# Kernel tuning notes

Measured on AMD Instinct MI355X. Metric: run time of the kernel, lower is better.

The kernel has to match this reference:

```python
import jax, jax.numpy as jnp
import numpy as np

NUM_CLASSES = 5
FEATURES = 256      # self.features_num
DIRECTIONS = 10000  # self.directions_num
H = 128
W = 128
LOSS_WEIGHT = 1.0


def setup_inputs() -> dict:
    key = jax.random.key(0)
    k1, k2, k3 = jax.random.split(key, 3)
    feature = jax.random.normal(k1, (1, FEATURES, H, W), dtype=jnp.float32)
    label = jax.random.randint(k2, (1, 1, H, W), 0, NUM_CLASSES, dtype=jnp.int32)
    proj_mat = jax.random.normal(k3, (DIRECTIONS, FEATURES), dtype=jnp.float32)
    # __init__ normalizes each row to unit norm
    proj_mat = proj_mat / jnp.sqrt((proj_mat ** 2).sum(axis=1, keepdims=True))
    return {"feature": feature, "label": label, "proj_mat": proj_mat}


def _class_loss(feat2d, w, proj_mat):
    # feat2d: [F, N] features, w: [N] {0,1} mask for this class, proj_mat: [D, F]
    n = w.sum()
    n_safe = jnp.maximum(n, 1.0)
    # first/second moments over the masked pixels (detached in the original via .cpu().numpy())
    miu = (feat2d @ w) / n_safe                                  # [F]
    m2mat = ((feat2d * w[None, :]) @ feat2d.T) / n_safe          # [F, F]
    cov_eps = jnp.clip(1e-8 * 1000.0 / n_safe, 1e-8, 1e-5)
    cov = m2mat - jnp.outer(miu, miu) + cov_eps * jnp.eye(FEATURES, dtype=feat2d.dtype)
    cov = jax.lax.stop_gradient(cov)  # original computes eig on detached numpy cov
    evals, evecs = jnp.linalg.eigh(cov)  # cov symmetric -> eigh (original: np.linalg.eig + sort)
    order = jnp.argsort(evals)[::-1]
    evals = jnp.maximum(evals[order], 1e-12)
    evecs = evecs[:, order]
    # per-direction variance after projection; rows of proj_mat already unit norm
    pm = proj_mat / jnp.sqrt((proj_mat ** 2).sum(axis=1, keepdims=True))
    std = jnp.sqrt((pm ** 2) @ evals)                            # [D]
    centered = feat2d - jax.lax.stop_gradient(miu)[:, None]      # miu_curr_t is detached
    # feat_vecs = proj_mat @ (evecs.T @ centered) / std  -> [D, N], the big intermediate
    fp = ((pm @ evecs.T) @ centered) / std[:, None]
    # masked moment accumulation (only class pixels contribute)
    m2 = ((fp ** 2) @ w) / n_safe                                # [D]
    m4 = ((fp ** 4) @ w) / n_safe                                # [D]
    loss_m2 = jnp.mean((m2 - 1.0) ** 2)
    loss_kurt = jnp.mean((m4 - 3.0 * m2 ** 2) ** 2)  # Gaussian target: m4 = 3*m2^2
    active = (n > 0).astype(feat2d.dtype)
    return loss_m2, loss_kurt, active


def reference(feature, label, proj_mat):
    feat2d = feature[0].reshape(FEATURES, H * W)    # [F, N]
    lbl = label[0, 0].reshape(H * W)                # [N]
    total = jnp.zeros((), dtype=feature.dtype)
    active_num = jnp.zeros((), dtype=feature.dtype)
    for c in range(1, NUM_CLASSES):  # original skips class 0 (background)
        w = (lbl == c).astype(feature.dtype)
        lm2, lk, a = _class_loss(feat2d, w, proj_mat)
        total = total + a * (lm2 + lk)
        active_num = active_num + a
    return LOSS_WEIGHT * total / jnp.maximum(active_num, 1.0)
```

## Files before the change

kernel.cpp:

```cpp
#include <hip/hip_runtime.h>
#include <cstdint>
#include <cstddef>

#define FEAT 256
#define HWPX 16384
#define NDIR 10000
#define NCLS 4
#define BCAP 4096
#define NSWO 7
#define JTOL 4e-12f
#define NBLK_FP 157

static const size_t OFF_FEATT = 0;
static const size_t OFF_IDX   = OFF_FEATT + (size_t)HWPX*FEAT;
static const size_t OFF_CNT   = OFF_IDX + (size_t)NCLS*HWPX;
static const size_t OFF_MIU   = OFF_CNT + 64;
static const size_t OFF_MIUP  = OFF_MIU + (size_t)NCLS*FEAT;
static const size_t OFF_G     = OFF_MIUP + (size_t)32*NCLS*FEAT;
static const size_t OFF_ETS   = OFF_G + (size_t)NCLS*FEAT*FEAT;
static const size_t OFF_EVAL  = OFF_ETS + (size_t)NCLS*FEAT*FEAT;
static const size_t OFF_LPART = OFF_EVAL + (size_t)NCLS*FEAT;
static const size_t OFF_B     = OFF_LPART + (size_t)NCLS*160*2;
static const size_t OFF_XCH   = OFF_B + (size_t)NCLS*FEAT*BCAP;

#define XCH_STRIDE ((size_t)2*32*2048)
#define XCH_XQ_OFF   16384
#define XCH_CSQ_OFF  32768
#define XCH_FLG_OFF  33280

__device__ __forceinline__ float wsum64(float v){
  int x;
  x = __builtin_amdgcn_update_dpp(0, __float_as_int(v), 0x121, 0xF, 0xF, false); v += __int_as_float(x);
  x = __builtin_amdgcn_update_dpp(0, __float_as_int(v), 0x122, 0xF, 0xF, false); v += __int_as_float(x);
  x = __builtin_amdgcn_update_dpp(0, __float_as_int(v), 0x124, 0xF, 0xF, false); v += __int_as_float(x);
  x = __builtin_amdgcn_update_dpp(0, __float_as_int(v), 0x128, 0xF, 0xF, false); v += __int_as_float(x);
  float a = __int_as_float(__builtin_amdgcn_readlane(__float_as_int(v), 0));
  float b = __int_as_float(__builtin_amdgcn_readlane(__float_as_int(v), 16));
  float c = __int_as_float(__builtin_amdgcn_readlane(__float_as_int(v), 32));
  float d = __int_as_float(__builtin_amdgcn_readlane(__float_as_int(v), 48));
  return (a + b) + (c + d);
}

__device__ __forceinline__ void waitflag(int* f, int val){
  while (__hip_atomic_load(f, __ATOMIC_ACQUIRE, __HIP_MEMORY_SCOPE_AGENT) < val)
    __builtin_amdgcn_s_sleep(2);
}

__global__ __launch_bounds__(256) void k_transpose(const float* __restrict__ feat, float* __restrict__ ws){
  __shared__ float tile[32][33];
  float* featT = ws + OFF_FEATT;
  int j0 = blockIdx.x*32, f0 = blockIdx.y*32;
  int tx = threadIdx.x, ty = threadIdx.y;
  #pragma unroll
  for (int r=0;r<4;r++){
    int f = f0 + ty + r*8;
    tile[ty+r*8][tx] = feat[(size_t)f*HWPX + j0 + tx];
  }
  __syncthreads();
  #pragma unroll
  for (int r=0;r<4;r++){
    int j = j0 + ty + r*8;
    featT[(size_t)j*FEAT + f0 + tx] = tile[tx][ty+r*8];
  }
}

__global__ __launch_bounds__(256) void k_index(const int* __restrict__ lab, float* ws){
  __shared__ int sc[256];
  int* idx = (int*)(ws + OFF_IDX);
  int* cnt = (int*)(ws + OFF_CNT);
  int t = threadIdx.x;
  if (t < NCLS*16){
    int cc = t >> 4, ii = t & 15;
    ((int*)(ws + OFF_XCH + (size_t)cc*XCH_STRIDE + XCH_FLG_OFF))[ii] = 0;
  }
  int base = t*64;
  for (int c=1;c<=NCLS;c++){
    __syncthreads();
    int m = 0;
    for (int k=0;k<64;k++) m += (lab[base+k]==c) ? 1 : 0;
    sc[t] = m;
    __syncthreads();
    for (int off=1; off<256; off<<=1){
      int v = (t>=off)? sc[t-off] : 0;
      __syncthreads();
      sc[t] += v;
      __syncthreads();
    }
    int pos = sc[t] - m;
    if (t==255) cnt[c-1] = sc[255];
    int* ic = idx + (size_t)(c-1)*HWPX;
    for (int k=0;k<64;k++){
      if (lab[base+k]==c) ic[pos++] = base+k;
    }
  }
}

__global__ __launch_bounds__(256) void k_miu_part(const int* __restrict__ lab, float* ws){
  const float* featT = ws + OFF_FEATT;
  float* part = ws + OFF_MIUP;
  int f = threadIdx.x;
  int b = blockIdx.x;
  int j0 = b*512;
  float a0=0.f,a1=0.f,a2=0.f,a3=0.f;
  for (int j=j0;j<j0+512;j++){
    float v = featT[(size_t)j*FEAT + f];
    int c = lab[j];
    a0 += (c==1)? v : 0.f;
    a1 += (c==2)? v : 0.f;
    a2 += (c==3)? v : 0.f;
    a3 += (c==4)? v : 0.f;
  }
  float* pb = part + (size_t)b*NCLS*FEAT;
  pb[0*FEAT+f] = a0;
  pb[1*FEAT+f] = a1;
  pb[2*FEAT+f] = a2;
  pb[3*FEAT+f] = a3;
}

__global__ __launch_bounds__(1024) void k_miu_fin(float* ws){
  int t = threadIdx.x;
  int c = t / FEAT;
  const float* part = ws + OFF_MIUP;
  float s = 0.f;
  for (int b=0;b<32;b++) s += part[(size_t)b*NCLS*FEAT + t];
  int n = ((int*)(ws+OFF_CNT))[c];
  float nf = fmaxf((float)n, 1.f);
  ws[OFF_MIU + t] = s / nf;
}

__global__ __launch_bounds__(256) void k_cov(float* ws){
  __shared__ float Xa[32][68];
  __shared__ float Xb[32][68];
  const float* featT = ws + OFF_FEATT;
  int c = blockIdx.y;
  const int* idx = (const int*)(ws + OFF_IDX) + (size_t)c*HWPX;
  int n = ((int*)(ws+OFF_CNT))[c];
  float nf = fmaxf((float)n,1.f);
  const float* miu = ws + OFF_MIU + (size_t)c*FEAT;
  float* G = ws + OFF_G + (size_t)c*FEAT*FEAT;
  int fb = (blockIdx.x & 3)*64, gb = (blockIdx.x >> 2)*64;
  int t = threadIdx.x;
  int ti = t & 15, tj = t >> 4;
  float acc[4][4] = {};
  int jr = t >> 3;
  int s8 = (t & 7) * 8;
  int nch = (n + 31)/32;
  for (int ch=0; ch<nch; ch++){
    int jg = ch*32 + jr;
    __syncthreads();
    if (jg < n){
      int jx = idx[jg];
      const float* row = featT + (size_t)jx*FEAT;
      #pragma unroll
      for (int k=0;k<8;k++){ Xa[jr][s8+k] = row[fb+s8+k]; Xb[jr][s8+k] = row[gb+s8+k]; }
    } else {
      #pragma unroll
      for (int k=0;k<8;k++){ Xa[jr][s8+k] = 0.f; Xb[jr][s8+k] = 0.f; }
    }
    __syncthreads();
    for (int jj=0;jj<32;jj++){
      float4 av = *(const float4*)&Xa[jj][ti*4];
      float4 bv = *(const float4*)&Xb[jj][tj*4];
      float aa[4] = {av.x,av.y,av.z,av.w};
      float bb[4] = {bv.x,bv.y,bv.z,bv.w};
      #pragma unroll
      for (int ii=0; ii<4; ii++)
        #pragma unroll
        for (int j2=0; j2<4; j2++)
          acc[ii][j2] += aa[ii]*bb[j2];
    }
  }
  float eps = fminf(fmaxf(1e-5f/nf, 1e-8f), 1e-5f);
  #pragma unroll
  for (int ii=0; ii<4; ii++){
    #pragma unroll
    for (int j2=0; j2<4; j2++){
      int f = fb + ti*4 + ii, g = gb + tj*4 + j2;
      float v = acc[ii][j2]/nf - miu[f]*miu[g] + ((f==g)? eps : 0.f);
      G[(size_t)g*FEAT + f] = v;
    }
  }
}

__global__ void
__attribute__((amdgpu_flat_work_group_size(256,256), amdgpu_waves_per_eu(1)))
k_jacobi(float* ws){
  __shared__ float QS[5*2048];
  __shared__ float PX[2][3*2048];
  __shared__ float colsq[256];
  __shared__ int srt[256];
  __shared__ int inv_[256];
  int c  = blockIdx.y;
  int kg = blockIdx.x;
  float* G   = ws + OFF_G + (size_t)c*FEAT*FEAT;
  float* XCH = ws + OFF_XCH + (size_t)c*XCH_STRIDE;
  float* XP  = XCH;
  float* XQ  = XCH + XCH_XQ_OFF;
  float* csqg= XCH + XCH_CSQ_OFF;
  int*   flg = (int*)(XCH + XCH_FLG_OFF);
  int t = threadIdx.x;
  int lane = t & 63;
  int lane4 = lane*4;
  int lw = t >> 6;
  int W  = kg*4 + lw;

#define FORJ8L(M) M(0) M(1) M(2) M(3) M(4) M(5) M(6) M(7)
#define FORJ8H(M) M(8) M(9) M(10) M(11) M(12) M(13) M(14) M(15)

#define DECL(j) float C##j##x, C##j##y, C##j##z, C##j##w;
  FORJ8L(DECL)
#undef DECL
  float n0,n1,n2,n3,n4,n5,n6,n7,n8,n9,n10,n11,n12,n13,n14,n15;

  int pg = (W==0)? 31 : W;
  int qg = (W==0)? 0  : 31 - W;

  int qslot = lw;
  int freeslot = 4;
  int qbase = qslot*2048 + lane4;

#define LDP(j) { float4 v_ = *(const float4*)&G[(size_t)(pg*8+(j))*FEAT + lane4]; \
                 C##j##x=v_.x; C##j##y=v_.y; C##j##z=v_.z; C##j##w=v_.w; }
  FORJ8L(LDP)
#undef LDP
#define LDQ(j) { float4 v_ = *(const float4*)&G[(size_t)(qg*8+((j)-8))*FEAT + lane4]; \
                 *(float4*)&QS[qbase + ((j)-8)*256] = v_; }
  FORJ8H(LDQ)
#undef LDQ

#define RP(g,ax,ay,az,aw) ax=C##g##x; ay=C##g##y; az=C##g##z; aw=C##g##w;
#define WP(g,ax,ay,az,aw) C##g##x=ax; C##g##y=ay; C##g##z=az; C##g##w=aw;
#define RQ(g,ax,ay,az,aw) { const float4 q_ = *(const float4*)&QS[qbase + ((g)-8)*256]; \
                            ax=q_.x; ay=q_.y; az=q_.z; aw=q_.w; }
#define WQ(g,ax,ay,az,aw) { float4 q_; q_.x=ax; q_.y=ay; q_.z=az; q_.w=aw; \
                            *(float4*)&QS[qbase + ((g)-8)*256] = q_; }

#define NRMP(j) n##j = wsum64(C##j##x*C##j##x + C##j##y*C##j##y + C##j##z*C##j##z + C##j##w*C##j##w);
#define NRMQ(j) { float ax,ay,az,aw; RQ(j,ax,ay,az,aw) \
                  n##j = wsum64(ax*ax + ay*ay + az*az + aw*aw); }

#define ROTG(LA,SA,ga,LB,SB,gb) { \
    float ax,ay,az,aw,bx,by,bz,bw; \
    LA(ga,ax,ay,az,aw) \
    LB(gb,bx,by,bz,bw) \
    float dp = ax*bx + ay*by + az*bz + aw*bw; \
    float d = wsum64(dp); \
    float na = n##ga, nb = n##gb; \
    bool doit = (d*d > na*nb*JTOL); \
    float tau = (nb - na) * 0.5f * __builtin_amdgcn_rcpf(d); \
    float tt = copysignf(__builtin_amdgcn_rcpf(fabsf(tau) + __builtin_amdgcn_sqrtf(1.f + tau*tau)), tau); \
    float cc = __builtin_amdgcn_rsqf(1.f + tt*tt); \
    float sn = tt*cc; \
    cc = doit ? cc : 1.f; \
    sn = doit ? sn : 0.f; \
    float x_; \
    x_ = ax; ax = cc*x_ - sn*bx; bx = sn*x_ + cc*bx; \
    x_ = ay; ay = cc*x_ - sn*by; by = sn*x_ + cc*by; \
    x_ = az; az = cc*x_ - sn*bz; bz = sn*x_ + cc*bz; \
    x_ = aw; aw = cc*x_ - sn*bw; bw = sn*x_ + cc*bw; \
    float cc2 = cc*cc, sn2 = sn*sn, csd = 2.f*cc*sn*d; \
    n##ga = cc2*na - csd + sn2*nb; \
    n##gb = sn2*na + csd + cc2*nb; \
    SA(ga,ax,ay,az,aw) \
    SB(gb,bx,by,bz,bw) \
  }
#define ROT_PP(a,b) ROTG(RP,WP,a,RP,WP,b)
#define ROT_PQ(a,b) ROTG(RP,WP,a,RQ,WQ,b)
#define ROT_QQ(a,b) ROTG(RQ,WQ,a,RQ,WQ,b)

#pragma clang loop unroll(disable)
  for (int R=0; R<NSWO*31; R++){
    NRMP(0) NRMP(1) NRMP(2) NRMP(3) NRMP(4) NRMP(5) NRMP(6) NRMP(7)
    NRMQ(8) NRMQ(9) NRMQ(10) NRMQ(11) NRMQ(12) NRMQ(13) NRMQ(14) NRMQ(15)
    ROT_PQ(0,8)  ROT_PQ(1,9)  ROT_PQ(2,10) ROT_PQ(3,11) ROT_PQ(4,12) ROT_PQ(5,13) ROT_PQ(6,14) ROT_PQ(7,15)
    ROT_PQ(0,9)  ROT_PQ(1,10) ROT_PQ(2,11) ROT_PQ(3,12) ROT_PQ(4,13) ROT_PQ(5,14) ROT_PQ(6,15) ROT_PQ(7,8)
    ROT_PQ(0,10) ROT_PQ(1,11) ROT_PQ(2,12) ROT_PQ(3,13) ROT_PQ(4,14) ROT_PQ(5,15) ROT_PQ(6,8)  ROT_PQ(7,9)
    ROT_PQ(0,11) ROT_PQ(1,12) ROT_PQ(2,13) ROT_PQ(3,14) ROT_PQ(4,15) ROT_PQ(5,8)  ROT_PQ(6,9)  ROT_PQ(7,10)
    ROT_PQ(0,12) ROT_PQ(1,13) ROT_PQ(2,14) ROT_PQ(3,15) ROT_PQ(4,8)  ROT_PQ(5,9)  ROT_PQ(6,10) ROT_PQ(7,11)
    ROT_PQ(0,13) ROT_PQ(1,14) ROT_PQ(2,15) ROT_PQ(3,8)  ROT_PQ(4,9)  ROT_PQ(5,10) ROT_PQ(6,11) ROT_PQ(7,12)
    ROT_PQ(0,14) ROT_PQ(1,15) ROT_PQ(2,8)  ROT_PQ(3,9)  ROT_PQ(4,10) ROT_PQ(5,11) ROT_PQ(6,12) ROT_PQ(7,13)
    ROT_PQ(0,15) ROT_PQ(1,8)  ROT_PQ(2,9)  ROT_PQ(3,10) ROT_PQ(4,11) ROT_PQ(5,12) ROT_PQ(6,13) ROT_PQ(7,14)
    if ((R & 3) == 3){
      ROT_PP(7,0) ROT_PP(1,6) ROT_PP(2,5) ROT_PP(3,4)  ROT_QQ(15,8)  ROT_QQ(9,14)  ROT_QQ(10,13) ROT_QQ(11,12)
      ROT_PP(7,1) ROT_PP(2,0) ROT_PP(3,6) ROT_PP(4,5)  ROT_QQ(15,9)  ROT_QQ(10,8)  ROT_QQ(11,14) ROT_QQ(12,13)
      ROT_PP(7,2) ROT_PP(3,1) ROT_PP(4,0) ROT_PP(5,6)  ROT_QQ(15,10) ROT_QQ(11,9)  ROT_QQ(12,8)  ROT_QQ(13,14)
      ROT_PP(7,3) ROT_PP(4,2) ROT_PP(5,1) ROT_PP(6,0)  ROT_QQ(15,11) ROT_QQ(12,10) ROT_QQ(13,9)  ROT_QQ(14,8)
      ROT_PP(7,4) ROT_PP(5,3) ROT_PP(6,2) ROT_PP(0,1)  ROT_QQ(15,12) ROT_QQ(13,11) ROT_QQ(14,10) ROT_QQ(8,9)
      ROT_PP(7,5) ROT_PP(6,4) ROT_PP(0,3) ROT_PP(1,2)  ROT_QQ(15,13) ROT_QQ(14,12) ROT_QQ(8,11)  ROT_QQ(9,10)
      ROT_PP(7,6) ROT_PP(0,5) ROT_PP(1,4) ROT_PP(2,3)  ROT_QQ(15,14) ROT_QQ(8,13)  ROT_QQ(9,12)  ROT_QQ(10,11)
    }

    int par = R & 1;
    if (lw >= 1){
      float* px = &PX[par][(lw-1)*2048];
#define STPX(j) { float4 v_; v_.x=C##j##x; v_.y=C##j##y; v_.z=C##j##z; v_.w=C##j##w; \
                  *(float4*)&px[(j)*256 + lane4] = v_; }
      FORJ8L(STPX)
#undef STPX
    }
    if (kg == 0 && lw == 1){
      int fb_ = freeslot*2048 + lane4;
#define STF(j) { float4 v_; v_.x=C##j##x; v_.y=C##j##y; v_.z=C##j##z; v_.w=C##j##w; \
                 *(float4*)&QS[fb_ + (j)*256] = v_; }
      FORJ8L(STF)
#undef STF
    }
    if (kg >= 1 && lw == 0){
      float* xp = XP + (size_t)(kg*2+par)*2048;
#define STXP(j) { float4 v_; v_.x=C##j##x; v_.y=C##j##y; v_.z=C##j##z; v_.w=C##j##w; \
                  *(float4*)&xp[(j)*256 + lane4] = v_; }
      FORJ8L(STXP)
#undef STXP
      if (lane == 0) __hip_atomic_store(&flg[kg], R+1, __ATOMIC_RELEASE, __HIP_MEMORY_SCOPE_AGENT);
    }
    if (lw == 3){
      if (kg < 3){
        float* xq = XQ + (size_t)(kg*2+par)*2048;
#define STXQ(j) { const float4 q_ = *(const float4*)&QS[qbase + (j)*256]; \
                  *(float4*)&xq[(j)*256 + lane4] = q_; }
        FORJ8L(STXQ)
#undef STXQ
        if (lane == 0) __hip_atomic_store(&flg[4+kg], R+1, __ATOMIC_RELEASE, __HIP_MEMORY_SCOPE_AGENT);
      } else {
#define LPQ(j) { const float4 q_ = *(const float4*)&QS[qbase + (j)*256]; \
                 C##j##x=q_.x; C##j##y=q_.y; C##j##z=q_.z; C##j##w=q_.w; }
        FORJ8L(LPQ)
#undef LPQ
      }
    }
    __syncthreads();
    if (lw <= 2 && W != 0){
      const float* px = &PX[par][lw*2048];
#define LDPX(j) { float4 v_ = *(const float4*)&px[(j)*256 + lane4]; \
                  C##j##x=v_.x; C##j##y=v_.y; C##j##z=v_.z; C##j##w=v_.w; }
      FORJ8L(LDPX)
#undef LDPX
    }
    if (lw == 3 && kg < 3){
      waitflag(&flg[kg+1], R+1);
      const float* xp = XP + (size_t)((kg+1)*2+par)*2048;
#define LDXP(j) { float4 v_ = *(const float4*)&xp[(j)*256 + lane4]; \
                  C##j##x=v_.x; C##j##y=v_.y; C##j##z=v_.z; C##j##w=v_.w; }
      FORJ8L(LDXP)
#undef LDXP
    }
    if (lw == 0 && kg >= 1){
      waitflag(&flg[4+kg-1], R+1);
      const float* xq = XQ + (size_t)((kg-1)*2+par)*2048;
      int fb_ = freeslot*2048 + lane4;
#define LDXQ(j) { float4 v_ = *(const float4*)&xq[(j)*256 + lane4]; \
                  *(float4*)&QS[fb_ + (j)*256] = v_; }
      FORJ8L(LDXQ)
#undef LDXQ
    }
    qslot += 4; if (qslot >= 5) qslot -= 5;
    freeslot += 4; if (freeslot >= 5) freeslot -= 5;
    qbase = qslot*2048 + lane4;
  }

  NRMP(0) NRMP(1) NRMP(2) NRMP(3) NRMP(4) NRMP(5) NRMP(6) NRMP(7)
  NRMQ(8) NRMQ(9) NRMQ(10) NRMQ(11) NRMQ(12) NRMQ(13) NRMQ(14) NRMQ(15)
#define WCS(j) if (lane == ((j)&15)) csqg[((j)<8)? (pg*8+(j)) : (qg*8+(j)-8)] = n##j;
  FORJ8L(WCS) FORJ8H(WCS)
#undef WCS
  __syncthreads();
  if (t == 0) __hip_atomic_fetch_add(&flg[8], 1, __ATOMIC_ACQ_REL, __HIP_MEMORY_SCOPE_AGENT);
  while (__hip_atomic_load(&flg[8], __ATOMIC_ACQUIRE, __HIP_MEMORY_SCOPE_AGENT) < 4)
    __builtin_amdgcn_s_sleep(2);
  colsq[t] = csqg[t];
  __syncthreads();
  {
    float my = colsq[t];
    int rk = 0;
    for (int u=0; u<256; u++){
      float cu = colsq[u];
      rk += ((cu > my) || (cu == my && u < t)) ? 1 : 0;
    }
    srt[rk] = t;
  }
  __syncthreads();
  float* evals = ws + OFF_EVAL + (size_t)c*FEAT;
  if (kg == 0) evals[t] = sqrtf(colsq[srt[t]]);
  inv_[srt[t]] = t;
  __syncthreads();
  float* Et = ws + OFF_ETS + (size_t)c*FEAT*FEAT;
#define WETP(j) { \
    int rk = inv_[pg*8+(j)]; \
    float iv = 1.f / sqrtf(n##j); \
    float4 v_; v_.x=C##j##x*iv; v_.y=C##j##y*iv; v_.z=C##j##z*iv; v_.w=C##j##w*iv; \
    *(float4*)&Et[(size_t)rk*FEAT + lane4] = v_; \
  }
  FORJ8L(WETP)
#undef WETP
#define WETQ(j) { \
    int rk = inv_[qg*8+(j)-8]; \
    float iv = 1.f / sqrtf(n##j); \
    const float4 q_ = *(const float4*)&QS[qbase + ((j)-8)*256]; \
    float4 v_; v_.x=q_.x*iv; v_.y=q_.y*iv; v_.z=q_.z*iv; v_.w=q_.w*iv; \
    *(float4*)&Et[(size_t)rk*FEAT + lane4] = v_; \
  }
  FORJ8H(WETQ)
#undef WETQ
#undef ROT_PP
#undef ROT_PQ
#undef ROT_QQ
#undef ROTG
#undef NRMP
#undef NRMQ
#undef RP
#undef WP
#undef RQ
#undef WQ
#undef FORJ8L
#undef FORJ8H
}

__global__ __launch_bounds__(256) void k_bmat(float* ws){
  __shared__ float Ae[256][68];
  __shared__ float Bc[256][68];
  int c = blockIdx.z;
  int n = ((int*)(ws+OFF_CNT))[c];
  int j0 = blockIdx.x*64;
  if (j0 >= n) return;
  int kb = blockIdx.y*64;
  const float* featT = ws + OFF_FEATT;
  const int* idx = (const int*)(ws + OFF_IDX) + (size_t)c*HWPX;
  const float* miu = ws + OFF_MIU + (size_t)c*FEAT;
  const float* Ets = ws + OFF_ETS + (size_t)c*FEAT*FEAT;
  float* Bg = ws + OFF_B + (size_t)c*FEAT*BCAP;
  int t = threadIdx.x;
  int l4 = t >> 2, sgf = (t & 3)*64;
  {
    const float* Erow = Ets + (size_t)(kb+l4)*FEAT + sgf;
    for (int f=0; f<64; f+=4){
      float4 v = *(const float4*)&Erow[f];
      Ae[sgf+f+0][l4] = v.x; Ae[sgf+f+1][l4] = v.y;
      Ae[sgf+f+2][l4] = v.z; Ae[sgf+f+3][l4] = v.w;
    }
  }
  {
    int jg = j0 + l4;
    if (jg < n){
      const float* Frow = featT + (size_t)idx[jg]*FEAT + sgf;
      const float* mp = miu + sgf;
      for (int f=0; f<64; f+=4){
        float4 v = *(const float4*)&Frow[f];
        Bc[sgf+f+0][l4] = v.x - mp[f+0];
        Bc[sgf+f+1][l4] = v.y - mp[f+1];
        Bc[sgf+f+2][l4] = v.z - mp[f+2];
        Bc[sgf+f+3][l4] = v.w - mp[f+3];
      }
    } else {
      for (int f=0; f<64; f++) Bc[sgf+f][l4] = 0.f;
    }
  }
  __syncthreads();
  int ti = t & 15, tj = t >> 4;
  float acc[4][4] = {};
  for (int f=0; f<FEAT; f+=4){
    #pragma unroll
    for (int ff=0; ff<4; ff++){
      float4 av = *(const float4*)&Ae[f+ff][ti*4];
      float4 bv = *(const float4*)&Bc[f+ff][tj*4];
      float aa[4] = {av.x,av.y,av.z,av.w};
      float bb[4] = {bv.x,bv.y,bv.z,bv.w};
      #pragma unroll
      for (int kk=0;kk<4;kk++)
        #pragma unroll
        for (int jj=0;jj<4;jj++)
          acc[kk][jj] += aa[kk]*bb[jj];
    }
  }
  #pragma unroll
  for (int kk=0; kk<4; kk++){
    float4 o; o.x=acc[kk][0]; o.y=acc[kk][1]; o.z=acc[kk][2]; o.w=acc[kk][3];
    *(float4*)&Bg[(size_t)(kb + ti*4 + kk)*BCAP + j0 + tj*4] = o;
  }
}

__global__ __launch_bounds__(256) void k_fp(const float* __restrict__ pm, float* ws){
  __shared__ float As[256][68];
  __shared__ float Bs[256][68];
  __shared__ float ev[256];
  __shared__ float red[64][17];
  __shared__ float m2s[64];
  __shared__ float m4s[64];
  int c = blockIdx.y;
  int i0 = blockIdx.x*64;
  int n = ((int*)(ws+OFF_CNT))[c];
  float nf = fmaxf((float)n, 1.f);
  const float* evals = ws + OFF_EVAL + (size_t)c*FEAT;
  const float* Bg = ws + OFF_B + (size_t)c*FEAT*BCAP;
  int t = threadIdx.x;
  int l4 = t >> 2;
  {
    int sgf = (t & 3)*64;
    int gi = i0 + l4;
    if (gi < NDIR){
      const float* row = pm + (size_t)gi*FEAT + sgf;
      for (int f=0; f<64; f+=4){
        float4 v = *(const float4*)&row[f];
        As[sgf+f+0][l4] = v.x; As[sgf+f+1][l4] = v.y;
        As[sgf+f+2][l4] = v.z; As[sgf+f+3][l4] = v.w;
      }
    } else {
      for (int f=0; f<64; f++) As[sgf+f][l4] = 0.f;
    }
  }
  if (t < 256) ev[t] = evals[t];
  int ti = t & 15, tj = t >> 4;
  float s2[4] = {0.f,0.f,0.f,0.f};
  float s4[4] = {0.f,0.f,0.f,0.f};
  int nch = (n + 63)/64;
  int sgj = (t & 3)*16;
  for (int ch=0; ch<nch; ch++){
    int j0 = ch*64;
    __syncthreads();
    for (int g=0; g<4; g++){
      int r = l4 + 64*g;
      const float* Brow = Bg + (size_t)r*BCAP + j0 + sgj;
      #pragma unroll
      for (int e=0; e<16; e+=4){
        int j = j0 + sgj + e;
        float4 v;
        if (j + 3 < n) v = *(const float4*)&Brow[e];
        else {
          v.x = (j+0<n)? Brow[e+0] : 0.f;
          v.y = (j+1<n)? Brow[e+1] : 0.f;
          v.z = (j+2<n)? Brow[e+2] : 0.f;
          v.w = (j+3<n)? Brow[e+3] : 0.f;
        }
        *(float4*)&Bs[r][sgj+e] = v;
      }
    }
    __syncthreads();
    float acc[4][4] = {};
    for (int k=0; k<FEAT; k+=4){
      #pragma unroll
      for (int kk=0; kk<4; kk++){
        float4 av = *(const float4*)&As[k+kk][ti*4];
        float4 bv = *(const float4*)&Bs[k+kk][tj*4];
        float aa[4] = {av.x,av.y,av.z,av.w};
        float bb[4] = {bv.x,bv.y,bv.z,bv.w};
        #pragma unroll
        for (int ii=0;ii<4;ii++)
          #pragma unroll
          for (int jj=0;jj<4;jj++)
            acc[ii][jj] += aa[ii]*bb[jj];
      }
    }
    #pragma unroll
    for (int ii=0;ii<4;ii++){
      #pragma unroll
      for (int jj=0;jj<4;jj++){
        float v = acc[ii][jj];
        float v2 = v*v;
        s2[ii] += v2;
        s4[ii] += v2*v2;
      }
    }
  }
  __syncthreads();
  #pragma unroll
  for (int ii=0;ii<4;ii++) red[ti*4+ii][tj] = s2[ii];
  __syncthreads();
  if (t < 64){
    float s = 0.f;
    for (int u=0;u<16;u++) s += red[t][u];
    m2s[t] = s;
  }
  __syncthreads();
  #pragma unroll
  for (int ii=0;ii<4;ii++) red[ti*4+ii][tj] = s4[ii];
  __syncthreads();
  if (t < 64){
    float s = 0.f;
    for (int u=0;u<16;u++) s += red[t][u];
    m4s[t] = s;
  }
  __syncthreads();
  if (t < 64){
    float stds = 0.f;
    for (int k=0;k<FEAT;k++){
      float a = As[k][t];
      stds += a*a*ev[k];
    }
    int i = i0 + t;
    float l2 = 0.f, lk = 0.f;
    if (i < NDIR){
      float m2 = m2s[t]/(nf*stds);
      float m4 = m4s[t]/(nf*stds*stds);
      float d2 = m2 - 1.f;
      l2 = d2*d2;
      float dk = m4 - 3.f*m2*m2;
      lk = dk*dk;
    }
    #pragma unroll
    for (int o=1;o<64;o<<=1){
      l2 += __shfl_xor(l2, o);
      lk += __shfl_xor(lk, o);
    }
    if (t == 0){
      float* lp = ws + OFF_LPART + ((size_t)c*160 + blockIdx.x)*2;
      lp[0] = l2;
      lp[1] = lk;
    }
  }
}

__global__ __launch_bounds__(64) void k_final(float* ws, float* out){
  int t = threadIdx.x;
  const int* cnt = (const int*)(ws + OFF_CNT);
  const float* lp = ws + OFF_LPART;
  float tot = 0.f, an = 0.f;
  for (int c=0;c<NCLS;c++){
    float s2 = 0.f, sk = 0.f;
    for (int b=t; b<NBLK_FP; b+=64){
      s2 += lp[((size_t)c*160 + b)*2 + 0];
      sk += lp[((size_t)c*160 + b)*2 + 1];
    }
    #pragma unroll
    for (int o=1;o<64;o<<=1){
      s2 += __shfl_xor(s2, o);
      sk += __shfl_xor(sk, o);
    }
    if (cnt[c] > 0){
      tot += s2/(float)NDIR + sk/(float)NDIR;
      an += 1.f;
    }
  }
  if (t == 0) out[0] = tot / fmaxf(an, 1.f);
}

extern "C" void kernel_launch(void* const* d_in, const int* in_sizes, int n_in,
                              void* d_out, int out_size, void* d_ws, size_t ws_size,
                              hipStream_t stream) {
  const float* feat = (const float*)d_in[0];
  const int*   lab  = (const int*)d_in[1];
  const float* pm   = (const float*)d_in[2];
  float* out = (float*)d_out;
  float* ws  = (float*)d_ws;

  hipLaunchKernelGGL(k_transpose, dim3(HWPX/32, FEAT/32), dim3(32,8), 0, stream, feat, ws);
  hipLaunchKernelGGL(k_index,     dim3(1),            dim3(256),     0, stream, lab, ws);
  hipLaunchKernelGGL(k_miu_part,  dim3(32),           dim3(256),     0, stream, lab, ws);
  hipLaunchKernelGGL(k_miu_fin,   dim3(1),            dim3(1024),    0, stream, ws);
  hipLaunchKernelGGL(k_cov,       dim3(16, NCLS),     dim3(256),     0, stream, ws);
  hipLaunchKernelGGL(k_jacobi,    dim3(4, NCLS),      dim3(256),     0, stream, ws);
  hipLaunchKernelGGL(k_bmat,      dim3(BCAP/64, 4, NCLS), dim3(256), 0, stream, ws);
  hipLaunchKernelGGL(k_fp,        dim3(NBLK_FP, NCLS), dim3(256),    0, stream, pm, ws);
  hipLaunchKernelGGL(k_final,     dim3(1),            dim3(64),      0, stream, ws, out);
}
```

Before: 4.585 ms.

## Split one-sided Jacobi across eight blocks per class with four-column groups

The one-sided Jacobi eigensolver now partitions the 256 columns into 64 groups of 4 instead of 32 groups of 8, and runs it on 8 blocks per class instead of 4. Each wave now holds fewer columns in registers and does fewer rotations per round, but needs twice as many rounds per sweep, with more cross-block flag handoffs. The goal is more parallelism and shorter per-round work on the serial eigen-decomposition. In exchange it adds inter-block synchronization and global exchange traffic, and spin-waiting blocks could deadlock if not all are co-resident.

```diff
diff --git a/kernel.cpp b/kernel.cpp
--- a/kernel.cpp
+++ b/kernel.cpp
@@ -69,8 +69,8 @@
   int* idx = (int*)(ws + OFF_IDX);
   int* cnt = (int*)(ws + OFF_CNT);
   int t = threadIdx.x;
-  if (t < NCLS*16){
-    int cc = t >> 4, ii = t & 15;
+  if (t < NCLS*32){
+    int cc = t >> 5, ii = t & 31;
     ((int*)(ws + OFF_XCH + (size_t)cc*XCH_STRIDE + XCH_FLG_OFF))[ii] = 0;
   }
   int base = t*64;
@@ -185,8 +185,8 @@
 __global__ void
 __attribute__((amdgpu_flat_work_group_size(256,256), amdgpu_waves_per_eu(1)))
 k_jacobi(float* ws){
-  __shared__ float QS[5*2048];
-  __shared__ float PX[2][3*2048];
+  __shared__ float QS[5*1024];
+  __shared__ float PX[2][3*1024];
   __shared__ float colsq[256];
   __shared__ int srt[256];
   __shared__ int inv_[256];
@@ -204,36 +204,36 @@
   int lw = t >> 6;
   int W  = kg*4 + lw;
 
-#define FORJ8L(M) M(0) M(1) M(2) M(3) M(4) M(5) M(6) M(7)
-#define FORJ8H(M) M(8) M(9) M(10) M(11) M(12) M(13) M(14) M(15)
+#define FORJ4L(M) M(0) M(1) M(2) M(3)
+#define FORJ4H(M) M(4) M(5) M(6) M(7)
 
 #define DECL(j) float C##j##x, C##j##y, C##j##z, C##j##w;
-  FORJ8L(DECL)
+  FORJ4L(DECL)
 #undef DECL
-  float n0,n1,n2,n3,n4,n5,n6,n7,n8,n9,n10,n11,n12,n13,n14,n15;
-
-  int pg = (W==0)? 31 : W;
-  int qg = (W==0)? 0  : 31 - W;
+  float n0,n1,n2,n3,n4,n5,n6,n7;
+
+  int pg = (W==0)? 63 : W;
+  int qg = (W==0)? 0  : 63 - W;
 
   int qslot = lw;
   int freeslot = 4;
-  int qbase = qslot*2048 + lane4;
-
-#define LDP(j) { float4 v_ = *(const float4*)&G[(size_t)(pg*8+(j))*FEAT + lane4]; \
+  int qbase = qslot*1024 + lane4;
+
+#define LDP(j) { float4 v_ = *(const float4*)&G[(size_t)(pg*4+(j))*FEAT + lane4]; \
                  C##j##x=v_.x; C##j##y=v_.y; C##j##z=v_.z; C##j##w=v_.w; }
-  FORJ8L(LDP)
+  FORJ4L(LDP)
 #undef LDP
-#define LDQ(j) { float4 v_ = *(const float4*)&G[(size_t)(qg*8+((j)-8))*FEAT + lane4]; \
-                 *(float4*)&QS[qbase + ((j)-8)*256] = v_; }
-  FORJ8H(LDQ)
+#define LDQ(j) { float4 v_ = *(const float4*)&G[(size_t)(qg*4+((j)-4))*FEAT + lane4]; \
+                 *(float4*)&QS[qbase + ((j)-4)*256] = v_; }
+  FORJ4H(LDQ)
 #undef LDQ
 
 #define RP(g,ax,ay,az,aw) ax=C##g##x; ay=C##g##y; az=C##g##z; aw=C##g##w;
 #define WP(g,ax,ay,az,aw) C##g##x=ax; C##g##y=ay; C##g##z=az; C##g##w=aw;
-#define RQ(g,ax,ay,az,aw) { const float4 q_ = *(const float4*)&QS[qbase + ((g)-8)*256]; \
+#define RQ(g,ax,ay,az,aw) { const float4 q_ = *(const float4*)&QS[qbase + ((g)-4)*256]; \
                             ax=q_.x; ay=q_.y; az=q_.z; aw=q_.w; }
 #define WQ(g,ax,ay,az,aw) { float4 q_; q_.x=ax; q_.y=ay; q_.z=az; q_.w=aw; \
-                            *(float4*)&QS[qbase + ((g)-8)*256] = q_; }
+                            *(float4*)&QS[qbase + ((g)-4)*256] = q_; }
 
 #define NRMP(j) n##j = wsum64(C##j##x*C##j##x + C##j##y*C##j##y + C##j##z*C##j##z + C##j##w*C##j##w);
 #define NRMQ(j) { float ax,ay,az,aw; RQ(j,ax,ay,az,aw) \
@@ -269,103 +269,95 @@
 #define ROT_QQ(a,b) ROTG(RQ,WQ,a,RQ,WQ,b)
 
 #pragma clang loop unroll(disable)
-  for (int R=0; R<NSWO*31; R++){
-    NRMP(0) NRMP(1) NRMP(2) NRMP(3) NRMP(4) NRMP(5) NRMP(6) NRMP(7)
-    NRMQ(8) NRMQ(9) NRMQ(10) NRMQ(11) NRMQ(12) NRMQ(13) NRMQ(14) NRMQ(15)
-    ROT_PQ(0,8)  ROT_PQ(1,9)  ROT_PQ(2,10) ROT_PQ(3,11) ROT_PQ(4,12) ROT_PQ(5,13) ROT_PQ(6,14) ROT_PQ(7,15)
-    ROT_PQ(0,9)  ROT_PQ(1,10) ROT_PQ(2,11) ROT_PQ(3,12) ROT_PQ(4,13) ROT_PQ(5,14) ROT_PQ(6,15) ROT_PQ(7,8)
-    ROT_PQ(0,10) ROT_PQ(1,11) ROT_PQ(2,12) ROT_PQ(3,13) ROT_PQ(4,14) ROT_PQ(5,15) ROT_PQ(6,8)  ROT_PQ(7,9)
-    ROT_PQ(0,11) ROT_PQ(1,12) ROT_PQ(2,13) ROT_PQ(3,14) ROT_PQ(4,15) ROT_PQ(5,8)  ROT_PQ(6,9)  ROT_PQ(7,10)
-    ROT_PQ(0,12) ROT_PQ(1,13) ROT_PQ(2,14) ROT_PQ(3,15) ROT_PQ(4,8)  ROT_PQ(5,9)  ROT_PQ(6,10) ROT_PQ(7,11)
-    ROT_PQ(0,13) ROT_PQ(1,14) ROT_PQ(2,15) ROT_PQ(3,8)  ROT_PQ(4,9)  ROT_PQ(5,10) ROT_PQ(6,11) ROT_PQ(7,12)
-    ROT_PQ(0,14) ROT_PQ(1,15) ROT_PQ(2,8)  ROT_PQ(3,9)  ROT_PQ(4,10) ROT_PQ(5,11) ROT_PQ(6,12) ROT_PQ(7,13)
-    ROT_PQ(0,15) ROT_PQ(1,8)  ROT_PQ(2,9)  ROT_PQ(3,10) ROT_PQ(4,11) ROT_PQ(5,12) ROT_PQ(6,13) ROT_PQ(7,14)
+  for (int R=0; R<NSWO*63; R++){
+    NRMP(0) NRMP(1) NRMP(2) NRMP(3)
+    NRMQ(4) NRMQ(5) NRMQ(6) NRMQ(7)
+    ROT_PQ(0,4) ROT_PQ(1,5) ROT_PQ(2,6) ROT_PQ(3,7)
+    ROT_PQ(0,5) ROT_PQ(1,6) ROT_PQ(2,7) ROT_PQ(3,4)
+    ROT_PQ(0,6) ROT_PQ(1,7) ROT_PQ(2,4) ROT_PQ(3,5)
+    ROT_PQ(0,7) ROT_PQ(1,4) ROT_PQ(2,5) ROT_PQ(3,6)
     if ((R & 3) == 3){
-      ROT_PP(7,0) ROT_PP(1,6) ROT_PP(2,5) ROT_PP(3,4)  ROT_QQ(15,8)  ROT_QQ(9,14)  ROT_QQ(10,13) ROT_QQ(11,12)
-      ROT_PP(7,1) ROT_PP(2,0) ROT_PP(3,6) ROT_PP(4,5)  ROT_QQ(15,9)  ROT_QQ(10,8)  ROT_QQ(11,14) ROT_QQ(12,13)
-      ROT_PP(7,2) ROT_PP(3,1) ROT_PP(4,0) ROT_PP(5,6)  ROT_QQ(15,10) ROT_QQ(11,9)  ROT_QQ(12,8)  ROT_QQ(13,14)
-      ROT_PP(7,3) ROT_PP(4,2) ROT_PP(5,1) ROT_PP(6,0)  ROT_QQ(15,11) ROT_QQ(12,10) ROT_QQ(13,9)  ROT_QQ(14,8)
-      ROT_PP(7,4) ROT_PP(5,3) ROT_PP(6,2) ROT_PP(0,1)  ROT_QQ(15,12) ROT_QQ(13,11) ROT_QQ(14,10) ROT_QQ(8,9)
-      ROT_PP(7,5) ROT_PP(6,4) ROT_PP(0,3) ROT_PP(1,2)  ROT_QQ(15,13) ROT_QQ(14,12) ROT_QQ(8,11)  ROT_QQ(9,10)
-      ROT_PP(7,6) ROT_PP(0,5) ROT_PP(1,4) ROT_PP(2,3)  ROT_QQ(15,14) ROT_QQ(8,13)  ROT_QQ(9,12)  ROT_QQ(10,11)
+      ROT_PP(3,0) ROT_PP(1,2)  ROT_QQ(7,4) ROT_QQ(5,6)
+      ROT_PP(3,1) ROT_PP(2,0)  ROT_QQ(7,5) ROT_QQ(6,4)
+      ROT_PP(3,2) ROT_PP(0,1)  ROT_QQ(7,6) ROT_QQ(4,5)
     }
 
     int par = R & 1;
     if (lw >= 1){
-      float* px = &PX[par][(lw-1)*2048];
+      float* px = &PX[par][(lw-1)*1024];
 #define STPX(j) { float4 v_; v_.x=C##j##x; v_.y=C##j##y; v_.z=C##j##z; v_.w=C##j##w; \
                   *(float4*)&px[(j)*256 + lane4] = v_; }
-      FORJ8L(STPX)
+      FORJ4L(STPX)
 #undef STPX
     }
     if (kg == 0 && lw == 1){
-      int fb_ = freeslot*2048 + lane4;
+      int fb_ = freeslot*1024 + lane4;
 #define STF(j) { float4 v_; v_.x=C##j##x; v_.y=C##j##y; v_.z=C##j##z; v_.w=C##j##w; \
                  *(float4*)&QS[fb_ + (j)*256] = v_; }
-      FORJ8L(STF)
+      FORJ4L(STF)
 #undef STF
     }
     if (kg >= 1 && lw == 0){
-      float* xp = XP + (size_t)(kg*2+par)*2048;
+      float* xp = XP + (size_t)(kg*2+par)*1024;
 #define STXP(j) { float4 v_; v_.x=C##j##x; v_.y=C##j##y; v_.z=C##j##z; v_.w=C##j##w; \
                   *(float4*)&xp[(j)*256 + lane4] = v_; }
-      FORJ8L(STXP)
+      FORJ4L(STXP)
 #undef STXP
       if (lane == 0) __hip_atomic_store(&flg[kg], R+1, __ATOMIC_RELEASE, __HIP_MEMORY_SCOPE_AGENT);
     }
     if (lw == 3){
-      if (kg < 3){
-        float* xq = XQ + (size_t)(kg*2+par)*2048;
+      if (kg < 7){
+        float* xq = XQ + (size_t)(kg*2+par)*1024;
 #define STXQ(j) { const float4 q_ = *(const float4*)&QS[qbase + (j)*256]; \
                   *(float4*)&xq[(j)*256 + lane4] = q_; }
-        FORJ8L(STXQ)
+        FORJ4L(STXQ)
 #undef STXQ
-        if (lane == 0) __hip_atomic_store(&flg[4+kg], R+1, __ATOMIC_RELEASE, __HIP_MEMORY_SCOPE_AGENT);
+        if (lane == 0) __hip_atomic_store(&flg[8+kg], R+1, __ATOMIC_RELEASE, __HIP_MEMORY_SCOPE_AGENT);
       } else {
 #define LPQ(j) { const float4 q_ = *(const float4*)&QS[qbase + (j)*256]; \
                  C##j##x=q_.x; C##j##y=q_.y; C##j##z=q_.z; C##j##w=q_.w; }
-        FORJ8L(LPQ)
+        FORJ4L(LPQ)
 #undef LPQ
       }
     }
     __syncthreads();
     if (lw <= 2 && W != 0){
-      const float* px = &PX[par][lw*2048];
+      const float* px = &PX[par][lw*1024];
 #define LDPX(j) { float4 v_ = *(const float4*)&px[(j)*256 + lane4]; \
                   C##j##x=v_.x; C##j##y=v_.y; C##j##z=v_.z; C##j##w=v_.w; }
-      FORJ8L(LDPX)
+      FORJ4L(LDPX)
 #undef LDPX
     }
-    if (lw == 3 && kg < 3){
+    if (lw == 3 && kg < 7){
       waitflag(&flg[kg+1], R+1);
-      const float* xp = XP + (size_t)((kg+1)*2+par)*2048;
+      const float* xp = XP + (size_t)((kg+1)*2+par)*1024;
 #define LDXP(j) { float4 v_ = *(const float4*)&xp[(j)*256 + lane4]; \
                   C##j##x=v_.x; C##j##y=v_.y; C##j##z=v_.z; C##j##w=v_.w; }
-      FORJ8L(LDXP)
+      FORJ4L(LDXP)
 #undef LDXP
     }
     if (lw == 0 && kg >= 1){
-      waitflag(&flg[4+kg-1], R+1);
-      const float* xq = XQ + (size_t)((kg-1)*2+par)*2048;
-      int fb_ = freeslot*2048 + lane4;
+      waitflag(&flg[8+kg-1], R+1);
+      const float* xq = XQ + (size_t)((kg-1)*2+par)*1024;
+      int fb_ = freeslot*1024 + lane4;
 #define LDXQ(j) { float4 v_ = *(const float4*)&xq[(j)*256 + lane4]; \
                   *(float4*)&QS[fb_ + (j)*256] = v_; }
-      FORJ8L(LDXQ)
+      FORJ4L(LDXQ)
 #undef LDXQ
     }
     qslot += 4; if (qslot >= 5) qslot -= 5;
     freeslot += 4; if (freeslot >= 5) freeslot -= 5;
-    qbase = qslot*2048 + lane4;
-  }
-
-  NRMP(0) NRMP(1) NRMP(2) NRMP(3) NRMP(4) NRMP(5) NRMP(6) NRMP(7)
-  NRMQ(8) NRMQ(9) NRMQ(10) NRMQ(11) NRMQ(12) NRMQ(13) NRMQ(14) NRMQ(15)
-#define WCS(j) if (lane == ((j)&15)) csqg[((j)<8)? (pg*8+(j)) : (qg*8+(j)-8)] = n##j;
-  FORJ8L(WCS) FORJ8H(WCS)
+    qbase = qslot*1024 + lane4;
+  }
+
+  NRMP(0) NRMP(1) NRMP(2) NRMP(3)
+  NRMQ(4) NRMQ(5) NRMQ(6) NRMQ(7)
+#define WCS(j) if (lane == (j)) csqg[((j)<4)? (pg*4+(j)) : (qg*4+(j)-4)] = n##j;
+  FORJ4L(WCS) FORJ4H(WCS)
 #undef WCS
   __syncthreads();
-  if (t == 0) __hip_atomic_fetch_add(&flg[8], 1, __ATOMIC_ACQ_REL, __HIP_MEMORY_SCOPE_AGENT);
-  while (__hip_atomic_load(&flg[8], __ATOMIC_ACQUIRE, __HIP_MEMORY_SCOPE_AGENT) < 4)
+  if (t == 0) __hip_atomic_fetch_add(&flg[16], 1, __ATOMIC_ACQ_REL, __HIP_MEMORY_SCOPE_AGENT);
+  while (__hip_atomic_load(&flg[16], __ATOMIC_ACQUIRE, __HIP_MEMORY_SCOPE_AGENT) < 8)
     __builtin_amdgcn_s_sleep(2);
   colsq[t] = csqg[t];
   __syncthreads();
@@ -385,21 +377,21 @@
   __syncthreads();
   float* Et = ws + OFF_ETS + (size_t)c*FEAT*FEAT;
 #define WETP(j) { \
-    int rk = inv_[pg*8+(j)]; \
+    int rk = inv_[pg*4+(j)]; \
     float iv = 1.f / sqrtf(n##j); \
     float4 v_; v_.x=C##j##x*iv; v_.y=C##j##y*iv; v_.z=C##j##z*iv; v_.w=C##j##w*iv; \
     *(float4*)&Et[(size_t)rk*FEAT + lane4] = v_; \
   }
-  FORJ8L(WETP)
+  FORJ4L(WETP)
 #undef WETP
 #define WETQ(j) { \
-    int rk = inv_[qg*8+(j)-8]; \
+    int rk = inv_[qg*4+(j)-4]; \
     float iv = 1.f / sqrtf(n##j); \
-    const float4 q_ = *(const float4*)&QS[qbase + ((j)-8)*256]; \
+    const float4 q_ = *(const float4*)&QS[qbase + ((j)-4)*256]; \
     float4 v_; v_.x=q_.x*iv; v_.y=q_.y*iv; v_.z=q_.z*iv; v_.w=q_.w*iv; \
     *(float4*)&Et[(size_t)rk*FEAT + lane4] = v_; \
   }
-  FORJ8H(WETQ)
+  FORJ4H(WETQ)
 #undef WETQ
 #undef ROT_PP
 #undef ROT_PQ
@@ -411,8 +403,8 @@
 #undef WP
 #undef RQ
 #undef WQ
-#undef FORJ8L
-#undef FORJ8H
+#undef FORJ4L
+#undef FORJ4H
 }
 
 __global__ __launch_bounds__(256) void k_bmat(float* ws){
@@ -646,7 +638,7 @@
   hipLaunchKernelGGL(k_miu_part,  dim3(32),           dim3(256),     0, stream, lab, ws);
   hipLaunchKernelGGL(k_miu_fin,   dim3(1),            dim3(1024),    0, stream, ws);
   hipLaunchKernelGGL(k_cov,       dim3(16, NCLS),     dim3(256),     0, stream, ws);
-  hipLaunchKernelGGL(k_jacobi,    dim3(4, NCLS),      dim3(256),     0, stream, ws);
+  hipLaunchKernelGGL(k_jacobi,    dim3(8, NCLS),      dim3(256),     0, stream, ws);
   hipLaunchKernelGGL(k_bmat,      dim3(BCAP/64, 4, NCLS), dim3(256), 0, stream, ws);
   hipLaunchKernelGGL(k_fp,        dim3(NBLK_FP, NCLS), dim3(256),    0, stream, pm, ws);
   hipLaunchKernelGGL(k_final,     dim3(1),            dim3(64),      0, stream, ws, out);
```

Measured after the change: 4.600 ms. No clear change (+0.3%).
